# Optimization experiments

Hardware: AMD Instinct MI355X
Metric: run time of the kernel (lower is better)

## Reference

```python
import jax, jax.numpy as jnp
import numpy as np

ALPHA = 0.95
TH_MIN = 0.4
TH_MAX = 1.5
LN_EPS = 1e-5
NORM_EPS = 1e-12


def setup_inputs() -> dict:
    key = jax.random.key(0)
    ks = jax.random.split(key, 8)
    B, L, H, V = 64, 2048, 128, 32000
    s = 1.0 / np.sqrt(H)
    return {
        "seq": jax.random.randint(ks[0], (B, L), 0, V),
        "embed": jax.random.normal(ks[1], (V, H), jnp.float32),
        "w1": jax.random.normal(ks[2], (H, 2 * H), jnp.float32) * s,
        "b1": jnp.zeros((2 * H,), jnp.float32),
        "w2": jax.random.normal(ks[3], (2 * H, H), jnp.float32) * (1.0 / np.sqrt(2 * H)),
        "b2": jnp.zeros((H,), jnp.float32),
        "ln_g": jnp.ones((H,), jnp.float32),
        "ln_b": jnp.zeros((H,), jnp.float32),
        "kp_w": jax.random.normal(ks[4], (H, H), jnp.float32) * s,
        "rp_w": jax.random.normal(ks[5], (H, H), jnp.float32) * s,
        "rp_b": jnp.zeros((H,), jnp.float32),
        "out_w": jax.random.normal(ks[6], (H, V), jnp.float32) * s,
        "out_b": jnp.zeros((V,), jnp.float32),
    }


def reference(seq, embed, w1, b1, w2, b2, ln_g, ln_b, kp_w, rp_w, rp_b, out_w, out_b):
    # Embedding + residual FFN + LayerNorm
    h = embed[seq]  # [B,L,H]
    x = h + (jnp.maximum(h @ w1 + b1, 0.0) @ w2 + b2)
    mu = jnp.mean(x, axis=-1, keepdims=True)
    var = jnp.mean(jnp.square(x - mu), axis=-1, keepdims=True)
    hn = (x - mu) * jax.lax.rsqrt(var + LN_EPS) * ln_g + ln_b
    B, L, H = hn.shape

    keys = hn @ kp_w  # [B,L,H] all projected keys (kp has no bias)
    ks_t = jnp.swapaxes(keys[:, :-1, :], 0, 1)  # [L-1,B,H] time-major for scan
    t_idx = jnp.arange(L - 1, dtype=hn.dtype)
    thresh = TH_MIN + (TH_MAX - TH_MIN) * (1.0 - t_idx / max(L - 1, 1))  # [L-1]

    def step(M, inputs):
        k, th = inputs  # k: [B,H], th: scalar
        kn = k / jnp.maximum(jnp.linalg.norm(k, axis=-1, keepdims=True), NORM_EPS)
        vp = jnp.einsum('bij,bj->bi', M, kn)  # predicted value
        err = k - vp
        fire = (jnp.linalg.norm(err, axis=-1) >= th * jnp.linalg.norm(k, axis=-1)).astype(M.dtype)
        delta = fire[:, None, None] * (err[:, :, None] * kn[:, None, :])  # gated outer product
        return M + (1.0 - ALPHA) * delta, None

    M0 = jnp.zeros((B, H, H), hn.dtype)
    M, _ = jax.lax.scan(step, M0, (ks_t, thresh))

    q = keys[:, -1, :]
    read = jnp.einsum('bij,bj->bi', M, q)
    return (read @ rp_w + rp_b) @ out_w + out_b
```

## Files before the change

### kernel.cpp

```cpp
#include <hip/hip_runtime.h>

#define HD 128
#define LD 2048
#define BD 64
#define VD 32000
#define NSTEP 2047

#define C_ALPHA  0.05f
#define C_THMIN  0.4f
#define C_THSPAN 1.1f
#define C_NEPS   1e-12f
#define C_LNEPS  1e-5f

#define HSP 132
#define W1P 68
#define W2P 132
#define ATP 68
#define TOK0 896
#define TBLK 9

extern "C" __global__ __launch_bounds__(512, 1)
void k_tokens(const int* __restrict__ seq, const float* __restrict__ embed,
              const float* __restrict__ w1, const float* __restrict__ b1,
              const float* __restrict__ w2, const float* __restrict__ b2,
              const float* __restrict__ lng, const float* __restrict__ lnb,
              const float* __restrict__ kp, float* __restrict__ keys)
{
  extern __shared__ float sm[];
  float* hs = sm;
  float* wt = sm + 128*HSP;
  float* at = wt + 128*W1P;
  const int tid = threadIdx.x;
  const int bb  = blockIdx.x / TBLK;
  const int rel = blockIdx.x % TBLK;
  const long long tokBase = (long long)bb * LD + TOK0 + rel * 128;

  for (int u = tid; u < 128*32; u += 512) {
    const int tok = u >> 5, seg = u & 31;
    const int s = seq[tokBase + tok];
    *(float4*)(hs + tok*HSP + seg*4) =
        *(const float4*)(embed + (long long)s*HD + seg*4);
  }
  __syncthreads();

  const int tg = tid >> 5;
  const int ig = tid & 31;

  float xacc[8][4] = {};

  for (int jt = 0; jt < 4; ++jt) {
    for (int u = tid; u < 128*16; u += 512) {
      const int i = u >> 4, q = u & 15;
      *(float4*)(wt + i*W1P + q*4) =
          *(const float4*)(w1 + (long long)i*256 + jt*64 + q*4);
    }
    __syncthreads();
    {
      float aa[8][2];
      float b1v[2];
      b1v[0] = b1[jt*64 + ig*2];
      b1v[1] = b1[jt*64 + ig*2 + 1];
      #pragma unroll
      for (int r = 0; r < 8; ++r) { aa[r][0] = b1v[0]; aa[r][1] = b1v[1]; }
      #pragma unroll 4
      for (int i4 = 0; i4 < 32; ++i4) {
        float2 wc[4];
        #pragma unroll
        for (int d = 0; d < 4; ++d)
          wc[d] = *(const float2*)(wt + (i4*4 + d)*W1P + ig*2);
        #pragma unroll
        for (int r = 0; r < 8; ++r) {
          float4 hv = *(const float4*)(hs + (tg + 16*r)*HSP + i4*4);
          aa[r][0] = fmaf(hv.x, wc[0].x, aa[r][0]);
          aa[r][0] = fmaf(hv.y, wc[1].x, aa[r][0]);
          aa[r][0] = fmaf(hv.z, wc[2].x, aa[r][0]);
          aa[r][0] = fmaf(hv.w, wc[3].x, aa[r][0]);
          aa[r][1] = fmaf(hv.x, wc[0].y, aa[r][1]);
          aa[r][1] = fmaf(hv.y, wc[1].y, aa[r][1]);
          aa[r][1] = fmaf(hv.z, wc[2].y, aa[r][1]);
          aa[r][1] = fmaf(hv.w, wc[3].y, aa[r][1]);
        }
      }
      #pragma unroll
      for (int r = 0; r < 8; ++r) {
        float2 o;
        o.x = fmaxf(aa[r][0], 0.0f);
        o.y = fmaxf(aa[r][1], 0.0f);
        *(float2*)(at + (tg + 16*r)*ATP + ig*2) = o;
      }
    }
    __syncthreads();
    for (int u = tid; u < 64*32; u += 512) {
      const int k = u >> 5, q = u & 31;
      *(float4*)(wt + k*W2P + q*4) =
          *(const float4*)(w2 + (long long)(jt*64 + k)*128 + q*4);
    }
    __syncthreads();
    #pragma unroll 2
    for (int k4 = 0; k4 < 16; ++k4) {
      float4 wr[4];
      #pragma unroll
      for (int d = 0; d < 4; ++d)
        wr[d] = *(const float4*)(wt + (k4*4 + d)*W2P + ig*4);
      #pragma unroll
      for (int r = 0; r < 8; ++r) {
        float4 av = *(const float4*)(at + (tg + 16*r)*ATP + k4*4);
        xacc[r][0] = fmaf(av.x, wr[0].x, xacc[r][0]);
        xacc[r][0] = fmaf(av.y, wr[1].x, xacc[r][0]);
        xacc[r][0] = fmaf(av.z, wr[2].x, xacc[r][0]);
        xacc[r][0] = fmaf(av.w, wr[3].x, xacc[r][0]);
        xacc[r][1] = fmaf(av.x, wr[0].y, xacc[r][1]);
        xacc[r][1] = fmaf(av.y, wr[1].y, xacc[r][1]);
        xacc[r][1] = fmaf(av.z, wr[2].y, xacc[r][1]);
        xacc[r][1] = fmaf(av.w, wr[3].y, xacc[r][1]);
        xacc[r][2] = fmaf(av.x, wr[0].z, xacc[r][2]);
        xacc[r][2] = fmaf(av.y, wr[1].z, xacc[r][2]);
        xacc[r][2] = fmaf(av.z, wr[2].z, xacc[r][2]);
        xacc[r][2] = fmaf(av.w, wr[3].z, xacc[r][2]);
        xacc[r][3] = fmaf(av.x, wr[0].w, xacc[r][3]);
        xacc[r][3] = fmaf(av.y, wr[1].w, xacc[r][3]);
        xacc[r][3] = fmaf(av.z, wr[2].w, xacc[r][3]);
        xacc[r][3] = fmaf(av.w, wr[3].w, xacc[r][3]);
      }
    }
    __syncthreads();
  }

  {
    float b2v[4], gv[4], bv[4];
    #pragma unroll
    for (int q = 0; q < 4; ++q) {
      b2v[q] = b2[ig*4 + q]; gv[q] = lng[ig*4 + q]; bv[q] = lnb[ig*4 + q];
    }
    #pragma unroll
    for (int r = 0; r < 8; ++r) {
      const int row = (tg + 16*r)*HSP + ig*4;
      float4 h0 = *(const float4*)(hs + row);
      float xr[4];
      xr[0] = h0.x + (xacc[r][0] + b2v[0]);
      xr[1] = h0.y + (xacc[r][1] + b2v[1]);
      xr[2] = h0.z + (xacc[r][2] + b2v[2]);
      xr[3] = h0.w + (xacc[r][3] + b2v[3]);
      float s = xr[0] + xr[1] + xr[2] + xr[3];
      s += __shfl_xor(s, 1, 32);  s += __shfl_xor(s, 2, 32);
      s += __shfl_xor(s, 4, 32);  s += __shfl_xor(s, 8, 32);
      s += __shfl_xor(s, 16, 32);
      const float mu = s * 0.0078125f;
      float vs = 0.0f;
      #pragma unroll
      for (int q = 0; q < 4; ++q) { float d = xr[q]-mu; vs = fmaf(d, d, vs); }
      vs += __shfl_xor(vs, 1, 32);  vs += __shfl_xor(vs, 2, 32);
      vs += __shfl_xor(vs, 4, 32);  vs += __shfl_xor(vs, 8, 32);
      vs += __shfl_xor(vs, 16, 32);
      const float rstd = 1.0f / sqrtf(vs * 0.0078125f + C_LNEPS);
      float4 o;
      o.x = (xr[0]-mu)*rstd*gv[0] + bv[0];
      o.y = (xr[1]-mu)*rstd*gv[1] + bv[1];
      o.z = (xr[2]-mu)*rstd*gv[2] + bv[2];
      o.w = (xr[3]-mu)*rstd*gv[3] + bv[3];
      *(float4*)(hs + row) = o;
    }
  }
  __syncthreads();

  {
    float ky[8][4] = {};
    for (int kt = 0; kt < 2; ++kt) {
      for (int u = tid; u < 64*32; u += 512) {
        const int k = u >> 5, q = u & 31;
        *(float4*)(wt + k*W2P + q*4) =
            *(const float4*)(kp + (long long)(kt*64 + k)*128 + q*4);
      }
      __syncthreads();
      #pragma unroll 2
      for (int k4 = 0; k4 < 16; ++k4) {
        float4 wr[4];
        #pragma unroll
        for (int d = 0; d < 4; ++d)
          wr[d] = *(const float4*)(wt + (k4*4 + d)*W2P + ig*4);
        #pragma unroll
        for (int r = 0; r < 8; ++r) {
          float4 hv = *(const float4*)(hs + (tg + 16*r)*HSP + kt*64 + k4*4);
          ky[r][0] = fmaf(hv.x, wr[0].x, ky[r][0]);
          ky[r][0] = fmaf(hv.y, wr[1].x, ky[r][0]);
          ky[r][0] = fmaf(hv.z, wr[2].x, ky[r][0]);
          ky[r][0] = fmaf(hv.w, wr[3].x, ky[r][0]);
          ky[r][1] = fmaf(hv.x, wr[0].y, ky[r][1]);
          ky[r][1] = fmaf(hv.y, wr[1].y, ky[r][1]);
          ky[r][1] = fmaf(hv.z, wr[2].y, ky[r][1]);
          ky[r][1] = fmaf(hv.w, wr[3].y, ky[r][1]);
          ky[r][2] = fmaf(hv.x, wr[0].z, ky[r][2]);
          ky[r][2] = fmaf(hv.y, wr[1].z, ky[r][2]);
          ky[r][2] = fmaf(hv.z, wr[2].z, ky[r][2]);
          ky[r][2] = fmaf(hv.w, wr[3].z, ky[r][2]);
          ky[r][3] = fmaf(hv.x, wr[0].w, ky[r][3]);
          ky[r][3] = fmaf(hv.y, wr[1].w, ky[r][3]);
          ky[r][3] = fmaf(hv.z, wr[2].w, ky[r][3]);
          ky[r][3] = fmaf(hv.w, wr[3].w, ky[r][3]);
        }
      }
      __syncthreads();
    }
    #pragma unroll
    for (int r = 0; r < 8; ++r) {
      const long long g = tokBase + tg + 16*r;
      float4 o;
      o.x = ky[r][0]; o.y = ky[r][1]; o.z = ky[r][2]; o.w = ky[r][3];
      *(float4*)(keys + g*HD + ig*4) = o;
    }
  }
}

#define C0 29
#define MSP 132
#define GPW 36
#define NT 768

#define INVB(buf,tok) Gxl[(tok)*GPW + 32 + (buf)]
#define TN2B(buf,tok) Gxl[(tok)*GPW + 34 + (buf)]

__device__ __forceinline__ float dpp_add_b1(float x){int y=__builtin_amdgcn_update_dpp(0,__float_as_int(x),0xB1,0xf,0xf,true);return x+__int_as_float(y);}
__device__ __forceinline__ float dpp_add_4e(float x){int y=__builtin_amdgcn_update_dpp(0,__float_as_int(x),0x4E,0xf,0xf,true);return x+__int_as_float(y);}
__device__ __forceinline__ float dpp_add_hm(float x){int y=__builtin_amdgcn_update_dpp(0,__float_as_int(x),0x141,0xf,0xf,true);return x+__int_as_float(y);}
__device__ __forceinline__ float dpp_add_mr(float x){int y=__builtin_amdgcn_update_dpp(0,__float_as_int(x),0x140,0xf,0xf,true);return x+__int_as_float(y);}
__device__ __forceinline__ float dpp_add_b15(float x){int y=__builtin_amdgcn_update_dpp(0,__float_as_int(x),0x142,0xf,0xf,true);return x+__int_as_float(y);}
__device__ __forceinline__ float dpp_add_b31(float x){int y=__builtin_amdgcn_update_dpp(0,__float_as_int(x),0x143,0xf,0xf,true);return x+__int_as_float(y);}

__device__ __forceinline__ void gram_half(const float* bufS, const float* bufT,
                                          float* dst, int half, int lane)
{
  const int sq = lane & 7, tq = lane >> 3;
  float ga[4][2] = {};
  for (int j4 = 0; j4 < 32; ++j4) {
    const int col = ((j4 + lane) & 31) * 4;
    float4 sv[4], tv[2];
    #pragma unroll
    for (int r = 0; r < 4; ++r)
      sv[r] = *(const float4*)(bufS + (sq + 8*r)*128 + col);
    #pragma unroll
    for (int q = 0; q < 2; ++q)
      tv[q] = *(const float4*)(bufT + (half*16 + tq*2 + q)*128 + col);
    #pragma unroll
    for (int r = 0; r < 4; ++r)
      #pragma unroll
      for (int q = 0; q < 2; ++q) {
        ga[r][q] = fmaf(sv[r].x, tv[q].x, ga[r][q]);
        ga[r][q] = fmaf(sv[r].y, tv[q].y, ga[r][q]);
        ga[r][q] = fmaf(sv[r].z, tv[q].z, ga[r][q]);
        ga[r][q] = fmaf(sv[r].w, tv[q].w, ga[r][q]);
      }
  }
  #pragma unroll
  for (int r = 0; r < 4; ++r)
    #pragma unroll
    for (int q = 0; q < 2; ++q)
      dst[(sq + 8*r)*GPW + half*16 + tq*2 + q] = ga[r][q];
}

extern "C" __global__ __launch_bounds__(768)
void k_scan(const float* __restrict__ keys,
            const float* __restrict__ rpw, const float* __restrict__ rpb,
            float* __restrict__ rr)
{
  extern __shared__ float sm[];
  float* Msh  = sm;
  float* kbuf = Msh + 128*MSP;
  float* PW   = kbuf + 3*4096;
  float* Gb   = PW + 2*4096;
  float* Gxl  = Gb + 2*32*GPW;

  const int tid  = threadIdx.x;
  const int lane = tid & 63;
  const int w    = tid >> 6;
  const int b    = blockIdx.x;
  const float* kb = keys + (long long)b * LD * HD;

  for (int u = tid; u < 128*MSP; u += NT) Msh[u] = 0.0f;
  for (int u = tid; u < 4096; u += NT) PW[(C0&1)*4096 + u] = 0.0f;
  {
    const int b30 = C0 % 3;
    for (int u = tid; u < 1024; u += NT)
      *(float4*)(kbuf + b30*4096 + u*4) =
          *(const float4*)(kb + (long long)(C0*32)*HD + u*4);
  }
  __syncthreads();
  {
    const float* kc = kbuf + (C0%3)*4096;
    for (int u = tid; u < 1024; u += NT) {
      const int s = u >> 5, t = u & 31;
      float a = 0.0f;
      for (int j4 = 0; j4 < 32; ++j4) {
        const int col = ((j4 + tid) & 31) * 4;
        float4 sv = *(const float4*)(kc + s*128 + col);
        float4 tv = *(const float4*)(kc + t*128 + col);
        a = fmaf(sv.x,tv.x,a); a = fmaf(sv.y,tv.y,a);
        a = fmaf(sv.z,tv.z,a); a = fmaf(sv.w,tv.w,a);
      }
      Gb[(C0&1)*32*GPW + s*GPW + t] = a;
    }
  }
  if (tid < 256) {
    const int tok = tid >> 3, pp = tid & 7;
    const float* kc = kbuf + (C0%3)*4096;
    float ss = 0.0f;
    #pragma unroll
    for (int q = 0; q < 4; ++q) {
      float4 v = *(const float4*)(kc + tok*128 + pp*16 + q*4);
      ss = fmaf(v.x,v.x,ss); ss = fmaf(v.y,v.y,ss);
      ss = fmaf(v.z,v.z,ss); ss = fmaf(v.w,v.w,ss);
    }
    ss += __shfl_xor(ss,1,8); ss += __shfl_xor(ss,2,8); ss += __shfl_xor(ss,4,8);
    if (pp == 0) {
      const float n = sqrtf(ss);
      INVB(C0&1, tok) = 1.0f / fmaxf(n, C_NEPS);
      const float th = C_THMIN + C_THSPAN * (1.0f - (float)(C0*32 + tok) / 2047.0f);
      const float tn = th * n;
      TN2B(C0&1, tok) = tn * tn;
    }
  }
  __syncthreads();

  for (int c = C0; c <= 64; ++c) {
    const int cur = c & 1, nxt = cur ^ 1;
    const int b3c = c % 3;
    const int b3n = (c + 1) % 3;
    const int b3p = (c + 2) % 3;
    const int t0 = c * 32;

    if (w < 8) {
      if (c > C0) {
        const int it = tid >> 5;
        const int jt = tid & 31;
        const int i0 = it*8, j0 = jt*4;
        const float* Wp  = PW + nxt*4096;
        const float* kfp = kbuf + b3p*4096;
        float acc[8][4] = {};
        for (int s = 0; s < 32; ++s) {
          const float4 wa = *(const float4*)(Wp + s*128 + i0);
          const float4 wb = *(const float4*)(Wp + s*128 + i0 + 4);
          const float4 k4 = *(const float4*)(kfp + s*128 + j0);
          float wv[8] = {wa.x,wa.y,wa.z,wa.w,wb.x,wb.y,wb.z,wb.w};
          float kv[4] = {k4.x,k4.y,k4.z,k4.w};
          #pragma unroll
          for (int a = 0; a < 8; ++a)
            #pragma unroll
            for (int q = 0; q < 4; ++q)
              acc[a][q] = fmaf(wv[a], kv[q], acc[a][q]);
        }
        #pragma unroll
        for (int a = 0; a < 8; ++a) {
          float* mp = Msh + (i0 + a)*MSP + j0;
          float4 m = *(float4*)mp;
          m.x = fmaf(C_ALPHA, acc[a][0], m.x);
          m.y = fmaf(C_ALPHA, acc[a][1], m.y);
          m.z = fmaf(C_ALPHA, acc[a][2], m.z);
          m.w = fmaf(C_ALPHA, acc[a][3], m.w);
          *(float4*)mp = m;
        }
      }
    } else {
      const int t2id = tid - 512;
      float4 kvl[4];
      if (c < 63) {
        #pragma unroll
        for (int q = 0; q < 4; ++q)
          kvl[q] = *(const float4*)(kb + (long long)(t0 + 32)*HD + (t2id + 256*q)*4);
      }
      if (c > C0 && c <= 63) {
        const int tt = t2id >> 5;
        const int i0 = (t2id & 31) * 4;
        const int tb4 = tt*4;
        const float* Wp = PW + nxt*4096;
        float fac[4][4] = {};
        for (int s = 0; s < 32; ++s) {
          const float4 gx = *(const float4*)(Gxl + s*GPW + tb4);
          const float4 wp = *(const float4*)(Wp + s*128 + i0);
          float gv[4] = {gx.x,gx.y,gx.z,gx.w};
          float pv[4] = {wp.x,wp.y,wp.z,wp.w};
          #pragma unroll
          for (int a = 0; a < 4; ++a)
            #pragma unroll
            for (int q = 0; q < 4; ++q)
              fac[a][q] = fmaf(gv[a], pv[q], fac[a][q]);
        }
        float* Pp = PW + cur*4096;
        #pragma unroll
        for (int a = 0; a < 4; ++a) {
          float* pp = Pp + (tb4 + a)*128 + i0;
          float4 p = *(float4*)pp;
          p.x = fmaf(C_ALPHA, fac[a][0], p.x);
          p.y = fmaf(C_ALPHA, fac[a][1], p.y);
          p.z = fmaf(C_ALPHA, fac[a][2], p.z);
          p.w = fmaf(C_ALPHA, fac[a][3], p.w);
          *(float4*)pp = p;
        }
      }
      if (c < 63) {
        #pragma unroll
        for (int q = 0; q < 4; ++q)
          *(float4*)(kbuf + b3n*4096 + (t2id + 256*q)*4) = kvl[q];
      }
    }
    __syncthreads();
    if (c == 64) break;

    if (w == 0) {
      __builtin_amdgcn_s_setprio(1);
      float* Pc = PW + cur*4096;
      const float* kfc = kbuf + b3c*4096;
      const float* Gc  = Gb + cur*32*GPW;
      const int l2 = lane*2;
      float2 acc[16];
      #pragma unroll
      for (int u = 0; u < 16; ++u) { acc[u].x = 0.0f; acc[u].y = 0.0f; }
      #pragma unroll
      for (int t = 0; t < 16; ++t) {
        const float2 p2 = *(const float2*)(Pc + t*128 + l2);
        const float2 k2 = *(const float2*)(kfc + t*128 + l2);
        const float it = INVB(cur, t);
        const float vx = it * fmaf(C_ALPHA, acc[t].x, p2.x);
        const float vy = it * fmaf(C_ALPHA, acc[t].y, p2.y);
        const float ex = k2.x - vx;
        const float ey = k2.y - vy;
        float e2 = fmaf(ex, ex, ey*ey);
        e2 = dpp_add_b1(e2); e2 = dpp_add_4e(e2);
        e2 = dpp_add_hm(e2); e2 = dpp_add_mr(e2);
        e2 = dpp_add_b15(e2); e2 = dpp_add_b31(e2);
        const float en2 = __int_as_float(__builtin_amdgcn_readlane(__float_as_int(e2), 63));
        const bool fire = (en2 >= TN2B(cur, t));
        const float wx = fire ? ex * it : 0.0f;
        const float wy = fire ? ey * it : 0.0f;
        float2 w2v; w2v.x = wx; w2v.y = wy;
        *(float2*)(Pc + t*128 + l2) = w2v;
        const float* gr = Gc + t*GPW;
        #pragma unroll
        for (int u4 = (t+1) & ~3; u4 < 16; u4 += 4) {
          const float4 g = *(const float4*)(gr + u4);
          acc[u4+0].x = fmaf(wx, g.x, acc[u4+0].x); acc[u4+0].y = fmaf(wy, g.x, acc[u4+0].y);
          acc[u4+1].x = fmaf(wx, g.y, acc[u4+1].x); acc[u4+1].y = fmaf(wy, g.y, acc[u4+1].y);
          acc[u4+2].x = fmaf(wx, g.z, acc[u4+2].x); acc[u4+2].y = fmaf(wy, g.z, acc[u4+2].y);
          acc[u4+3].x = fmaf(wx, g.w, acc[u4+3].x); acc[u4+3].y = fmaf(wy, g.w, acc[u4+3].y);
        }
      }
      #pragma unroll
      for (int u = 0; u < 16; ++u) { acc[u].x = 0.0f; acc[u].y = 0.0f; }
      #pragma unroll
      for (int s = 0; s < 16; ++s) {
        const float2 ws = *(const float2*)(Pc + s*128 + l2);
        const float* gs = Gc + s*GPW + 16;
        #pragma unroll
        for (int u4 = 0; u4 < 16; u4 += 4) {
          const float4 g = *(const float4*)(gs + u4);
          acc[u4+0].x = fmaf(ws.x, g.x, acc[u4+0].x); acc[u4+0].y = fmaf(ws.y, g.x, acc[u4+0].y);
          acc[u4+1].x = fmaf(ws.x, g.y, acc[u4+1].x); acc[u4+1].y = fmaf(ws.y, g.y, acc[u4+1].y);
          acc[u4+2].x = fmaf(ws.x, g.z, acc[u4+2].x); acc[u4+2].y = fmaf(ws.y, g.z, acc[u4+2].y);
          acc[u4+3].x = fmaf(ws.x, g.w, acc[u4+3].x); acc[u4+3].y = fmaf(ws.y, g.w, acc[u4+3].y);
        }
      }
      #pragma unroll
      for (int t = 16; t < 32; ++t) {
        const int tt = t - 16;
        const float2 p2 = *(const float2*)(Pc + t*128 + l2);
        const float2 k2 = *(const float2*)(kfc + t*128 + l2);
        const float it = INVB(cur, t);
        const float vx = it * fmaf(C_ALPHA, acc[tt].x, p2.x);
        const float vy = it * fmaf(C_ALPHA, acc[tt].y, p2.y);
        const float ex = k2.x - vx;
        const float ey = k2.y - vy;
        float e2 = fmaf(ex, ex, ey*ey);
        e2 = dpp_add_b1(e2); e2 = dpp_add_4e(e2);
        e2 = dpp_add_hm(e2); e2 = dpp_add_mr(e2);
        e2 = dpp_add_b15(e2); e2 = dpp_add_b31(e2);
        const float en2 = __int_as_float(__builtin_amdgcn_readlane(__float_as_int(e2), 63));
        const bool fire = (en2 >= TN2B(cur, t)) && (t0 + t < NSTEP);
        const float wx = fire ? ex * it : 0.0f;
        const float wy = fire ? ey * it : 0.0f;
        float2 w2v; w2v.x = wx; w2v.y = wy;
        *(float2*)(Pc + t*128 + l2) = w2v;
        const float* gr = Gc + t*GPW + 16;
        #pragma unroll
        for (int u4 = (tt+1) & ~3; u4 < 16; u4 += 4) {
          const float4 g = *(const float4*)(gr + u4);
          acc[u4+0].x = fmaf(wx, g.x, acc[u4+0].x); acc[u4+0].y = fmaf(wy, g.x, acc[u4+0].y);
          acc[u4+1].x = fmaf(wx, g.y, acc[u4+1].x); acc[u4+1].y = fmaf(wy, g.y, acc[u4+1].y);
          acc[u4+2].x = fmaf(wx, g.z, acc[u4+2].x); acc[u4+2].y = fmaf(wy, g.z, acc[u4+2].y);
          acc[u4+3].x = fmaf(wx, g.w, acc[u4+3].x); acc[u4+3].y = fmaf(wy, g.w, acc[u4+3].y);
        }
      }
      __builtin_amdgcn_s_setprio(0);
    } else if (c < 63) {
      int p;
      switch (w) {
        case 4:  p = 0; break;  case 8:  p = 1; break;
        case 1:  p = 2; break;  case 5:  p = 3; break;  case 9:  p = 4; break;
        case 2:  p = 5; break;  case 6:  p = 6; break;  case 10: p = 7; break;
        default: p = -1;
      }
      if (p >= 0) {
        const float* kfn = kbuf + b3n*4096;
        const int tb4 = p*4;
        const int ib = lane & 31, ih = lane >> 5;
        float pa[4][2] = {};
        for (int j4 = 0; j4 < 32; ++j4) {
          float4 kv[4], mv[2];
          #pragma unroll
          for (int ss = 0; ss < 4; ++ss)
            kv[ss] = *(const float4*)(kfn + (tb4+ss)*128 + j4*4);
          #pragma unroll
          for (int r = 0; r < 2; ++r)
            mv[r] = *(const float4*)(Msh + (ib + 32*(ih + 2*r))*MSP + j4*4);
          #pragma unroll
          for (int ss = 0; ss < 4; ++ss)
            #pragma unroll
            for (int r = 0; r < 2; ++r) {
              pa[ss][r] = fmaf(kv[ss].x, mv[r].x, pa[ss][r]);
              pa[ss][r] = fmaf(kv[ss].y, mv[r].y, pa[ss][r]);
              pa[ss][r] = fmaf(kv[ss].z, mv[r].z, pa[ss][r]);
              pa[ss][r] = fmaf(kv[ss].w, mv[r].w, pa[ss][r]);
            }
        }
        float* Pp = PW + nxt*4096;
        #pragma unroll
        for (int ss = 0; ss < 4; ++ss)
          #pragma unroll
          for (int r = 0; r < 2; ++r)
            Pp[(tb4+ss)*128 + ib + 32*(ih + 2*r)] = pa[ss][r];
        if (w == 4) {
          const float* kn = kbuf + b3n*4096;
          const int tok = lane >> 1, hh = lane & 1;
          float ss2 = 0.0f;
          #pragma unroll
          for (int q = 0; q < 16; ++q) {
            const int cq = (q + lane) & 15;
            float4 v = *(const float4*)(kn + tok*128 + hh*64 + cq*4);
            ss2 = fmaf(v.x,v.x,ss2); ss2 = fmaf(v.y,v.y,ss2);
            ss2 = fmaf(v.z,v.z,ss2); ss2 = fmaf(v.w,v.w,ss2);
          }
          ss2 += __shfl_xor(ss2, 1);
          if (hh == 0) {
            const float n = sqrtf(ss2);
            INVB(nxt, tok) = 1.0f / fmaxf(n, C_NEPS);
            const float th = C_THMIN + C_THSPAN * (1.0f - (float)(t0 + 32 + tok) / 2047.0f);
            const float tn = th * n;
            TN2B(nxt, tok) = tn * tn;
          }
        }
      } else if (w == 3) {
        gram_half(kbuf + b3n*4096, kbuf + b3n*4096, Gb + nxt*32*GPW, 0, lane);
      } else if (w == 7) {
        gram_half(kbuf + b3n*4096, kbuf + b3n*4096, Gb + nxt*32*GPW, 1, lane);
      } else {
        gram_half(kbuf + b3c*4096, kbuf + b3n*4096, Gxl, 0, lane);
        gram_half(kbuf + b3c*4096, kbuf + b3n*4096, Gxl, 1, lane);
      }
    }
    __syncthreads();
  }

  {
    float* qv = PW;
    float* rd = PW + 128;
    if (tid < 32)
      *(float4*)(qv + tid*4) =
          *(const float4*)(kb + (long long)(LD-1)*HD + tid*4);
    __syncthreads();
    if (tid < 512) {
      const int i = tid >> 2, p = tid & 3;
      const float* mr = Msh + i*MSP + p*32;
      const float* qp = qv + p*32;
      float a0 = 0.0f, a1 = 0.0f;
      #pragma unroll
      for (int q4 = 0; q4 < 8; q4 += 2) {
        const float4 m0 = *(const float4*)(mr + q4*4);
        const float4 m1 = *(const float4*)(mr + q4*4 + 4);
        a0 = fmaf(m0.x, qp[q4*4+0], a0); a0 = fmaf(m0.y, qp[q4*4+1], a0);
        a0 = fmaf(m0.z, qp[q4*4+2], a0); a0 = fmaf(m0.w, qp[q4*4+3], a0);
        a1 = fmaf(m1.x, qp[q4*4+4], a1); a1 = fmaf(m1.y, qp[q4*4+5], a1);
        a1 = fmaf(m1.z, qp[q4*4+6], a1); a1 = fmaf(m1.w, qp[q4*4+7], a1);
      }
      float acc = a0 + a1;
      acc += __shfl_xor(acc, 1);
      acc += __shfl_xor(acc, 2);
      if (p == 0) rd[i] = acc;
    }
    __syncthreads();
    if (tid < 128) {
      float s0 = rpb[tid], s1 = 0.0f, s2 = 0.0f, s3 = 0.0f;
      for (int k = 0; k < 128; k += 4) {
        s0 = fmaf(rd[k+0], rpw[(k+0)*128 + tid], s0);
        s1 = fmaf(rd[k+1], rpw[(k+1)*128 + tid], s1);
        s2 = fmaf(rd[k+2], rpw[(k+2)*128 + tid], s2);
        s3 = fmaf(rd[k+3], rpw[(k+3)*128 + tid], s3);
      }
      rr[b*128 + tid] = (s0 + s1) + (s2 + s3);
    }
  }
}

extern "C" __global__ __launch_bounds__(256, 1)
void k_out(const float* __restrict__ rr, const float* __restrict__ outw,
           const float* __restrict__ outb, float* __restrict__ out)
{
  __shared__ float rl[64*128];
  const int tid = threadIdx.x;
  for (int u = tid; u < 8192; u += 256) rl[u] = rr[u];
  __syncthreads();
  const int v  = blockIdx.x*64 + (tid & 63);
  const int bg = tid >> 6;
  const float ob = outb[v];
  const float* rbase = rl + bg*16*128;
  float acc[16];
  #pragma unroll
  for (int bb = 0; bb < 16; ++bb) acc[bb] = 0.0f;
  for (int h = 0; h < 128; h += 2) {
    const float wv0 = outw[(long long)h*VD + v];
    const float wv1 = outw[(long long)(h+1)*VD + v];
    #pragma unroll
    for (int bb = 0; bb < 16; ++bb) {
      acc[bb] = fmaf(rbase[bb*128 + h],     wv0, acc[bb]);
      acc[bb] = fmaf(rbase[bb*128 + h + 1], wv1, acc[bb]);
    }
  }
  #pragma unroll
  for (int bb = 0; bb < 16; ++bb)
    out[(long long)(bg*16 + bb)*VD + v] = acc[bb] + ob;
}

extern "C" void kernel_launch(void* const* d_in, const int* in_sizes, int n_in,
                              void* d_out, int out_size, void* d_ws, size_t ws_size,
                              hipStream_t stream)
{
  const int*   seq   = (const int*)d_in[0];
  const float* embed = (const float*)d_in[1];
  const float* w1    = (const float*)d_in[2];
  const float* b1    = (const float*)d_in[3];
  const float* w2    = (const float*)d_in[4];
  const float* b2    = (const float*)d_in[5];
  const float* ln_g  = (const float*)d_in[6];
  const float* ln_b  = (const float*)d_in[7];
  const float* kp_w  = (const float*)d_in[8];
  const float* rp_w  = (const float*)d_in[9];
  const float* rp_b  = (const float*)d_in[10];
  const float* out_w = (const float*)d_in[11];
  const float* out_b = (const float*)d_in[12];
  float* out = (float*)d_out;

  char* ws = (char*)d_ws;
  float* keys = (float*)ws;
  float* rr   = (float*)(ws + 67108864 + 4194304);

  hipLaunchKernelGGL(k_tokens, dim3(64*TBLK), dim3(512), 137216, stream,
                     seq, embed, w1, b1, w2, b2, ln_g, ln_b, kp_w, keys);
  hipLaunchKernelGGL(k_scan, dim3(64), dim3(768), 163328, stream,
                     keys, rp_w, rp_b, rr);
  hipLaunchKernelGGL(k_out, dim3(500), dim3(256), 0, stream, rr, out_w, out_b, out);
}
```

Measured before the change: 756.8 us.

## Fuse token producer and scan into one persistent kernel with flag-based handoff

```diff
diff --git a/kernel.cpp b/kernel.cpp
--- a/kernel.cpp
+++ b/kernel.cpp
@@ -17,51 +17,100 @@
 #define W2P 132
 #define ATP 68
 #define TOK0 896
-#define TBLK 9
-
-extern "C" __global__ __launch_bounds__(512, 1)
-void k_tokens(const int* __restrict__ seq, const float* __restrict__ embed,
-              const float* __restrict__ w1, const float* __restrict__ b1,
-              const float* __restrict__ w2, const float* __restrict__ b2,
-              const float* __restrict__ lng, const float* __restrict__ lnb,
-              const float* __restrict__ kp, float* __restrict__ keys)
+
+#define C0 29
+#define MSP 132
+#define GPW 36
+#define NT 768
+
+#define INVB(buf,tok) Gxl[(tok)*GPW + 32 + (buf)]
+#define TN2B(buf,tok) Gxl[(tok)*GPW + 34 + (buf)]
+
+__device__ __forceinline__ float dpp_add_b1(float x){int y=__builtin_amdgcn_update_dpp(0,__float_as_int(x),0xB1,0xf,0xf,true);return x+__int_as_float(y);}
+__device__ __forceinline__ float dpp_add_4e(float x){int y=__builtin_amdgcn_update_dpp(0,__float_as_int(x),0x4E,0xf,0xf,true);return x+__int_as_float(y);}
+__device__ __forceinline__ float dpp_add_hm(float x){int y=__builtin_amdgcn_update_dpp(0,__float_as_int(x),0x141,0xf,0xf,true);return x+__int_as_float(y);}
+__device__ __forceinline__ float dpp_add_mr(float x){int y=__builtin_amdgcn_update_dpp(0,__float_as_int(x),0x140,0xf,0xf,true);return x+__int_as_float(y);}
+__device__ __forceinline__ float dpp_add_b15(float x){int y=__builtin_amdgcn_update_dpp(0,__float_as_int(x),0x142,0xf,0xf,true);return x+__int_as_float(y);}
+__device__ __forceinline__ float dpp_add_b31(float x){int y=__builtin_amdgcn_update_dpp(0,__float_as_int(x),0x143,0xf,0xf,true);return x+__int_as_float(y);}
+
+__device__ __forceinline__ void wait_flag(int* flags, int idx) {
+  while (__hip_atomic_load(&flags[idx], __ATOMIC_ACQUIRE,
+                           __HIP_MEMORY_SCOPE_AGENT) == 0)
+    __builtin_amdgcn_s_sleep(16);
+}
+
+__device__ __forceinline__ void gram_half(const float* bufS, const float* bufT,
+                                          float* dst, int half, int lane)
 {
-  extern __shared__ float sm[];
+  const int sq = lane & 7, tq = lane >> 3;
+  float ga[4][2] = {};
+  for (int j4 = 0; j4 < 32; ++j4) {
+    const int col = ((j4 + lane) & 31) * 4;
+    float4 sv[4], tv[2];
+    #pragma unroll
+    for (int r = 0; r < 4; ++r)
+      sv[r] = *(const float4*)(bufS + (sq + 8*r)*128 + col);
+    #pragma unroll
+    for (int q = 0; q < 2; ++q)
+      tv[q] = *(const float4*)(bufT + (half*16 + tq*2 + q)*128 + col);
+    #pragma unroll
+    for (int r = 0; r < 4; ++r)
+      #pragma unroll
+      for (int q = 0; q < 2; ++q) {
+        ga[r][q] = fmaf(sv[r].x, tv[q].x, ga[r][q]);
+        ga[r][q] = fmaf(sv[r].y, tv[q].y, ga[r][q]);
+        ga[r][q] = fmaf(sv[r].z, tv[q].z, ga[r][q]);
+        ga[r][q] = fmaf(sv[r].w, tv[q].w, ga[r][q]);
+      }
+  }
+  #pragma unroll
+  for (int r = 0; r < 4; ++r)
+    #pragma unroll
+    for (int q = 0; q < 2; ++q)
+      dst[(sq + 8*r)*GPW + half*16 + tq*2 + q] = ga[r][q];
+}
+
+__device__ void produce_tile(int bb, int rel,
+                             const int* __restrict__ seq, const float* __restrict__ embed,
+                             const float* __restrict__ w1, const float* __restrict__ b1,
+                             const float* __restrict__ w2, const float* __restrict__ b2,
+                             const float* __restrict__ lng, const float* __restrict__ lnb,
+                             const float* __restrict__ kp, float* __restrict__ keys,
+                             float* sm, int tid)
+{
   float* hs = sm;
-  float* wt = sm + 128*HSP;
+  float* wt = sm + 64*HSP;
   float* at = wt + 128*W1P;
-  const int tid = threadIdx.x;
-  const int bb  = blockIdx.x / TBLK;
-  const int rel = blockIdx.x % TBLK;
-  const long long tokBase = (long long)bb * LD + TOK0 + rel * 128;
-
-  for (int u = tid; u < 128*32; u += 512) {
-    const int tok = u >> 5, seg = u & 31;
-    const int s = seq[tokBase + tok];
-    *(float4*)(hs + tok*HSP + seg*4) =
-        *(const float4*)(embed + (long long)s*HD + seg*4);
-  }
+  const long long tokBase = (long long)bb * LD + TOK0 + rel * 64;
+
+  if (tid < 512)
+    for (int u = tid; u < 64*32; u += 512) {
+      const int tok = u >> 5, seg = u & 31;
+      const int s = seq[tokBase + tok];
+      *(float4*)(hs + tok*HSP + seg*4) =
+          *(const float4*)(embed + (long long)s*HD + seg*4);
+    }
   __syncthreads();
 
-  const int tg = tid >> 5;
+  const int tg = (tid >> 5) & 15;
   const int ig = tid & 31;
-
-  float xacc[8][4] = {};
+  float xacc[4][4] = {};
 
   for (int jt = 0; jt < 4; ++jt) {
-    for (int u = tid; u < 128*16; u += 512) {
-      const int i = u >> 4, q = u & 15;
-      *(float4*)(wt + i*W1P + q*4) =
-          *(const float4*)(w1 + (long long)i*256 + jt*64 + q*4);
-    }
-    __syncthreads();
-    {
-      float aa[8][2];
+    if (tid < 512)
+      for (int u = tid; u < 128*16; u += 512) {
+        const int i = u >> 4, q = u & 15;
+        *(float4*)(wt + i*W1P + q*4) =
+            *(const float4*)(w1 + (long long)i*256 + jt*64 + q*4);
+      }
+    __syncthreads();
+    if (tid < 512) {
+      float aa[4][2];
       float b1v[2];
       b1v[0] = b1[jt*64 + ig*2];
       b1v[1] = b1[jt*64 + ig*2 + 1];
       #pragma unroll
-      for (int r = 0; r < 8; ++r) { aa[r][0] = b1v[0]; aa[r][1] = b1v[1]; }
+      for (int r = 0; r < 4; ++r) { aa[r][0] = b1v[0]; aa[r][1] = b1v[1]; }
       #pragma unroll 4
       for (int i4 = 0; i4 < 32; ++i4) {
         float2 wc[4];
@@ -69,7 +118,7 @@
         for (int d = 0; d < 4; ++d)
           wc[d] = *(const float2*)(wt + (i4*4 + d)*W1P + ig*2);
         #pragma unroll
-        for (int r = 0; r < 8; ++r) {
+        for (int r = 0; r < 4; ++r) {
           float4 hv = *(const float4*)(hs + (tg + 16*r)*HSP + i4*4);
           aa[r][0] = fmaf(hv.x, wc[0].x, aa[r][0]);
           aa[r][0] = fmaf(hv.y, wc[1].x, aa[r][0]);
@@ -82,7 +131,7 @@
         }
       }
       #pragma unroll
-      for (int r = 0; r < 8; ++r) {
+      for (int r = 0; r < 4; ++r) {
         float2 o;
         o.x = fmaxf(aa[r][0], 0.0f);
         o.y = fmaxf(aa[r][1], 0.0f);
@@ -90,50 +139,53 @@
       }
     }
     __syncthreads();
-    for (int u = tid; u < 64*32; u += 512) {
-      const int k = u >> 5, q = u & 31;
-      *(float4*)(wt + k*W2P + q*4) =
-          *(const float4*)(w2 + (long long)(jt*64 + k)*128 + q*4);
-    }
-    __syncthreads();
-    #pragma unroll 2
-    for (int k4 = 0; k4 < 16; ++k4) {
-      float4 wr[4];
-      #pragma unroll
-      for (int d = 0; d < 4; ++d)
-        wr[d] = *(const float4*)(wt + (k4*4 + d)*W2P + ig*4);
-      #pragma unroll
-      for (int r = 0; r < 8; ++r) {
-        float4 av = *(const float4*)(at + (tg + 16*r)*ATP + k4*4);
-        xacc[r][0] = fmaf(av.x, wr[0].x, xacc[r][0]);
-        xacc[r][0] = fmaf(av.y, wr[1].x, xacc[r][0]);
-        xacc[r][0] = fmaf(av.z, wr[2].x, xacc[r][0]);
-        xacc[r][0] = fmaf(av.w, wr[3].x, xacc[r][0]);
-        xacc[r][1] = fmaf(av.x, wr[0].y, xacc[r][1]);
-        xacc[r][1] = fmaf(av.y, wr[1].y, xacc[r][1]);
-        xacc[r][1] = fmaf(av.z, wr[2].y, xacc[r][1]);
-        xacc[r][1] = fmaf(av.w, wr[3].y, xacc[r][1]);
-        xacc[r][2] = fmaf(av.x, wr[0].z, xacc[r][2]);
-        xacc[r][2] = fmaf(av.y, wr[1].z, xacc[r][2]);
-        xacc[r][2] = fmaf(av.z, wr[2].z, xacc[r][2]);
-        xacc[r][2] = fmaf(av.w, wr[3].z, xacc[r][2]);
-        xacc[r][3] = fmaf(av.x, wr[0].w, xacc[r][3]);
-        xacc[r][3] = fmaf(av.y, wr[1].w, xacc[r][3]);
-        xacc[r][3] = fmaf(av.z, wr[2].w, xacc[r][3]);
-        xacc[r][3] = fmaf(av.w, wr[3].w, xacc[r][3]);
-      }
-    }
-    __syncthreads();
-  }
-
-  {
+    if (tid < 512)
+      for (int u = tid; u < 64*32; u += 512) {
+        const int k = u >> 5, q = u & 31;
+        *(float4*)(wt + k*W2P + q*4) =
+            *(const float4*)(w2 + (long long)(jt*64 + k)*128 + q*4);
+      }
+    __syncthreads();
+    if (tid < 512) {
+      #pragma unroll 2
+      for (int k4 = 0; k4 < 16; ++k4) {
+        float4 wr[4];
+        #pragma unroll
+        for (int d = 0; d < 4; ++d)
+          wr[d] = *(const float4*)(wt + (k4*4 + d)*W2P + ig*4);
+        #pragma unroll
+        for (int r = 0; r < 4; ++r) {
+          float4 av = *(const float4*)(at + (tg + 16*r)*ATP + k4*4);
+          xacc[r][0] = fmaf(av.x, wr[0].x, xacc[r][0]);
+          xacc[r][0] = fmaf(av.y, wr[1].x, xacc[r][0]);
+          xacc[r][0] = fmaf(av.z, wr[2].x, xacc[r][0]);
+          xacc[r][0] = fmaf(av.w, wr[3].x, xacc[r][0]);
+          xacc[r][1] = fmaf(av.x, wr[0].y, xacc[r][1]);
+          xacc[r][1] = fmaf(av.y, wr[1].y, xacc[r][1]);
+          xacc[r][1] = fmaf(av.z, wr[2].y, xacc[r][1]);
+          xacc[r][1] = fmaf(av.w, wr[3].y, xacc[r][1]);
+          xacc[r][2] = fmaf(av.x, wr[0].z, xacc[r][2]);
+          xacc[r][2] = fmaf(av.y, wr[1].z, xacc[r][2]);
+          xacc[r][2] = fmaf(av.z, wr[2].z, xacc[r][2]);
+          xacc[r][2] = fmaf(av.w, wr[3].z, xacc[r][2]);
+          xacc[r][3] = fmaf(av.x, wr[0].w, xacc[r][3]);
+          xacc[r][3] = fmaf(av.y, wr[1].w, xacc[r][3]);
+          xacc[r][3] = fmaf(av.z, wr[2].w, xacc[r][3]);
+          xacc[r][3] = fmaf(av.w, wr[3].w, xacc[r][3]);
+        }
+      }
+    }
+    __syncthreads();
+  }
+
+  if (tid < 512) {
     float b2v[4], gv[4], bv[4];
     #pragma unroll
     for (int q = 0; q < 4; ++q) {
       b2v[q] = b2[ig*4 + q]; gv[q] = lng[ig*4 + q]; bv[q] = lnb[ig*4 + q];
     }
     #pragma unroll
-    for (int r = 0; r < 8; ++r) {
+    for (int r = 0; r < 4; ++r) {
       const int row = (tg + 16*r)*HSP + ig*4;
       float4 h0 = *(const float4*)(hs + row);
       float xr[4];
@@ -164,112 +216,92 @@
   __syncthreads();
 
   {
-    float ky[8][4] = {};
+    float ky[4][4] = {};
     for (int kt = 0; kt < 2; ++kt) {
-      for (int u = tid; u < 64*32; u += 512) {
-        const int k = u >> 5, q = u & 31;
-        *(float4*)(wt + k*W2P + q*4) =
-            *(const float4*)(kp + (long long)(kt*64 + k)*128 + q*4);
-      }
+      if (tid < 512)
+        for (int u = tid; u < 64*32; u += 512) {
+          const int k = u >> 5, q = u & 31;
+          *(float4*)(wt + k*W2P + q*4) =
+              *(const float4*)(kp + (long long)(kt*64 + k)*128 + q*4);
+        }
       __syncthreads();
-      #pragma unroll 2
-      for (int k4 = 0; k4 < 16; ++k4) {
-        float4 wr[4];
-        #pragma unroll
-        for (int d = 0; d < 4; ++d)
-          wr[d] = *(const float4*)(wt + (k4*4 + d)*W2P + ig*4);
-        #pragma unroll
-        for (int r = 0; r < 8; ++r) {
-          float4 hv = *(const float4*)(hs + (tg + 16*r)*HSP + kt*64 + k4*4);
-          ky[r][0] = fmaf(hv.x, wr[0].x, ky[r][0]);
-          ky[r][0] = fmaf(hv.y, wr[1].x, ky[r][0]);
-          ky[r][0] = fmaf(hv.z, wr[2].x, ky[r][0]);
-          ky[r][0] = fmaf(hv.w, wr[3].x, ky[r][0]);
-          ky[r][1] = fmaf(hv.x, wr[0].y, ky[r][1]);
-          ky[r][1] = fmaf(hv.y, wr[1].y, ky[r][1]);
-          ky[r][1] = fmaf(hv.z, wr[2].y, ky[r][1]);
-          ky[r][1] = fmaf(hv.w, wr[3].y, ky[r][1]);
-          ky[r][2] = fmaf(hv.x, wr[0].z, ky[r][2]);
-          ky[r][2] = fmaf(hv.y, wr[1].z, ky[r][2]);
-          ky[r][2] = fmaf(hv.z, wr[2].z, ky[r][2]);
-          ky[r][2] = fmaf(hv.w, wr[3].z, ky[r][2]);
-          ky[r][3] = fmaf(hv.x, wr[0].w, ky[r][3]);
-          ky[r][3] = fmaf(hv.y, wr[1].w, ky[r][3]);
-          ky[r][3] = fmaf(hv.z, wr[2].w, ky[r][3]);
-          ky[r][3] = fmaf(hv.w, wr[3].w, ky[r][3]);
+      if (tid < 512) {
+        #pragma unroll 2
+        for (int k4 = 0; k4 < 16; ++k4) {
+          float4 wr[4];
+          #pragma unroll
+          for (int d = 0; d < 4; ++d)
+            wr[d] = *(const float4*)(wt + (k4*4 + d)*W2P + ig*4);
+          #pragma unroll
+          for (int r = 0; r < 4; ++r) {
+            float4 hv = *(const float4*)(hs + (tg + 16*r)*HSP + kt*64 + k4*4);
+            ky[r][0] = fmaf(hv.x, wr[0].x, ky[r][0]);
+            ky[r][0] = fmaf(hv.y, wr[1].x, ky[r][0]);
+            ky[r][0] = fmaf(hv.z, wr[2].x, ky[r][0]);
+            ky[r][0] = fmaf(hv.w, wr[3].x, ky[r][0]);
+            ky[r][1] = fmaf(hv.x, wr[0].y, ky[r][1]);
+            ky[r][1] = fmaf(hv.y, wr[1].y, ky[r][1]);
+            ky[r][1] = fmaf(hv.z, wr[2].y, ky[r][1]);
+            ky[r][1] = fmaf(hv.w, wr[3].y, ky[r][1]);
+            ky[r][2] = fmaf(hv.x, wr[0].z, ky[r][2]);
+            ky[r][2] = fmaf(hv.y, wr[1].z, ky[r][2]);
+            ky[r][2] = fmaf(hv.z, wr[2].z, ky[r][2]);
+            ky[r][2] = fmaf(hv.w, wr[3].z, ky[r][2]);
+            ky[r][3] = fmaf(hv.x, wr[0].w, ky[r][3]);
+            ky[r][3] = fmaf(hv.y, wr[1].w, ky[r][3]);
+            ky[r][3] = fmaf(hv.z, wr[2].w, ky[r][3]);
+            ky[r][3] = fmaf(hv.w, wr[3].w, ky[r][3]);
+          }
         }
       }
       __syncthreads();
     }
-    #pragma unroll
-    for (int r = 0; r < 8; ++r) {
-      const long long g = tokBase + tg + 16*r;
-      float4 o;
-      o.x = ky[r][0]; o.y = ky[r][1]; o.z = ky[r][2]; o.w = ky[r][3];
-      *(float4*)(keys + g*HD + ig*4) = o;
+    if (tid < 512) {
+      #pragma unroll
+      for (int r = 0; r < 4; ++r) {
+        const long long g = tokBase + tg + 16*r;
+        float4 o;
+        o.x = ky[r][0]; o.y = ky[r][1]; o.z = ky[r][2]; o.w = ky[r][3];
+        *(float4*)(keys + g*HD + ig*4) = o;
+      }
     }
   }
 }
 
-#define C0 29
-#define MSP 132
-#define GPW 36
-#define NT 768
-
-#define INVB(buf,tok) Gxl[(tok)*GPW + 32 + (buf)]
-#define TN2B(buf,tok) Gxl[(tok)*GPW + 34 + (buf)]
-
-__device__ __forceinline__ float dpp_add_b1(float x){int y=__builtin_amdgcn_update_dpp(0,__float_as_int(x),0xB1,0xf,0xf,true);return x+__int_as_float(y);}
-__device__ __forceinline__ float dpp_add_4e(float x){int y=__builtin_amdgcn_update_dpp(0,__float_as_int(x),0x4E,0xf,0xf,true);return x+__int_as_float(y);}
-__device__ __forceinline__ float dpp_add_hm(float x){int y=__builtin_amdgcn_update_dpp(0,__float_as_int(x),0x141,0xf,0xf,true);return x+__int_as_float(y);}
-__device__ __forceinline__ float dpp_add_mr(float x){int y=__builtin_amdgcn_update_dpp(0,__float_as_int(x),0x140,0xf,0xf,true);return x+__int_as_float(y);}
-__device__ __forceinline__ float dpp_add_b15(float x){int y=__builtin_amdgcn_update_dpp(0,__float_as_int(x),0x142,0xf,0xf,true);return x+__int_as_float(y);}
-__device__ __forceinline__ float dpp_add_b31(float x){int y=__builtin_amdgcn_update_dpp(0,__float_as_int(x),0x143,0xf,0xf,true);return x+__int_as_float(y);}
-
-__device__ __forceinline__ void gram_half(const float* bufS, const float* bufT,
-                                          float* dst, int half, int lane)
-{
-  const int sq = lane & 7, tq = lane >> 3;
-  float ga[4][2] = {};
-  for (int j4 = 0; j4 < 32; ++j4) {
-    const int col = ((j4 + lane) & 31) * 4;
-    float4 sv[4], tv[2];
-    #pragma unroll
-    for (int r = 0; r < 4; ++r)
-      sv[r] = *(const float4*)(bufS + (sq + 8*r)*128 + col);
-    #pragma unroll
-    for (int q = 0; q < 2; ++q)
-      tv[q] = *(const float4*)(bufT + (half*16 + tq*2 + q)*128 + col);
-    #pragma unroll
-    for (int r = 0; r < 4; ++r)
-      #pragma unroll
-      for (int q = 0; q < 2; ++q) {
-        ga[r][q] = fmaf(sv[r].x, tv[q].x, ga[r][q]);
-        ga[r][q] = fmaf(sv[r].y, tv[q].y, ga[r][q]);
-        ga[r][q] = fmaf(sv[r].z, tv[q].z, ga[r][q]);
-        ga[r][q] = fmaf(sv[r].w, tv[q].w, ga[r][q]);
-      }
-  }
-  #pragma unroll
-  for (int r = 0; r < 4; ++r)
-    #pragma unroll
-    for (int q = 0; q < 2; ++q)
-      dst[(sq + 8*r)*GPW + half*16 + tq*2 + q] = ga[r][q];
-}
-
 extern "C" __global__ __launch_bounds__(768)
-void k_scan(const float* __restrict__ keys,
+void k_main(const int* __restrict__ seq, const float* __restrict__ embed,
+            const float* __restrict__ w1, const float* __restrict__ b1,
+            const float* __restrict__ w2, const float* __restrict__ b2,
+            const float* __restrict__ lng, const float* __restrict__ lnb,
+            const float* __restrict__ kp, float* __restrict__ keys,
             const float* __restrict__ rpw, const float* __restrict__ rpb,
-            float* __restrict__ rr)
+            float* __restrict__ rr, int* flags)
 {
   extern __shared__ float sm[];
+  const int tid = threadIdx.x;
+
+  if (blockIdx.x >= 64) {
+    const int pb = blockIdx.x - 64;
+    for (int k = 0; k < 6; ++k) {
+      const int g = pb + 192*k;
+      const int rel = g >> 6, bb2 = g & 63;
+      produce_tile(bb2, rel, seq, embed, w1, b1, w2, b2, lng, lnb, kp,
+                   keys, sm, tid);
+      __syncthreads();
+      if (tid == 0)
+        __hip_atomic_store(&flags[g], 1, __ATOMIC_RELEASE,
+                           __HIP_MEMORY_SCOPE_AGENT);
+      __syncthreads();
+    }
+    return;
+  }
+
   float* Msh  = sm;
   float* kbuf = Msh + 128*MSP;
   float* PW   = kbuf + 3*4096;
   float* Gb   = PW + 2*4096;
   float* Gxl  = Gb + 2*32*GPW;
 
-  const int tid  = threadIdx.x;
   const int lane = tid & 63;
   const int w    = tid >> 6;
   const int b    = blockIdx.x;
@@ -277,6 +309,7 @@
 
   for (int u = tid; u < 128*MSP; u += NT) Msh[u] = 0.0f;
   for (int u = tid; u < 4096; u += NT) PW[(C0&1)*4096 + u] = 0.0f;
+  wait_flag(flags, b);
   {
     const int b30 = C0 % 3;
     for (int u = tid; u < 1024; u += NT)
@@ -326,6 +359,9 @@
     const int b3n = (c + 1) % 3;
     const int b3p = (c + 2) % 3;
     const int t0 = c * 32;
+
+    if (c < 63)
+      wait_flag(flags, ((t0 + 63 - 896) >> 6) * 64 + b);
 
     if (w < 8) {
       if (c > C0) {
@@ -648,10 +684,11 @@
   char* ws = (char*)d_ws;
   float* keys = (float*)ws;
   float* rr   = (float*)(ws + 67108864 + 4194304);
-
-  hipLaunchKernelGGL(k_tokens, dim3(64*TBLK), dim3(512), 137216, stream,
-                     seq, embed, w1, b1, w2, b2, ln_g, ln_b, kp_w, keys);
-  hipLaunchKernelGGL(k_scan, dim3(64), dim3(768), 163328, stream,
-                     keys, rp_w, rp_b, rr);
+  int*   flags = (int*)(ws + 67108864 + 4194304 + 65536);
+
+  hipMemsetAsync(flags, 0, 1152 * sizeof(int), stream);
+  hipLaunchKernelGGL(k_main, dim3(256), dim3(768), 163328, stream,
+                     seq, embed, w1, b1, w2, b2, ln_g, ln_b, kp_w,
+                     keys, rp_w, rp_b, rr, flags);
   hipLaunchKernelGGL(k_out, dim3(500), dim3(256), 0, stream, rr, out_w, out_b, out);
 }
```

Measured after the change: 636.5 us. -15.9%, faster.
